# Kernel tuning notes

Measured on AMD Instinct MI355X. Metric: run time of the kernel, lower is better.

## Reference

```python
import jax, jax.numpy as jnp
import numpy as np
import math

B, H, S, D = 2, 16, 2048, 128
COEFF = 2.0  # layer_number


def setup_inputs() -> dict:
    key = jax.random.key(0)
    kq, kk, kv = jax.random.split(key, 3)
    return {
        "query_layer": jax.random.normal(kq, (B, H, S, D), dtype=jnp.float32),
        "key_layer": jax.random.normal(kk, (B, H, S, D), dtype=jnp.float32),
        "value_layer": jax.random.normal(kv, (B, H, S, D), dtype=jnp.float32),
    }


def reference(query_layer, key_layer, value_layer):
    b, h, sq, d = query_layer.shape
    sk = key_layer.shape[2]
    norm_factor = math.sqrt(d) * COEFF
    # raw scores [b,h,sq,sk]; divide by sqrt(d)*coeff, cast fp32, multiply by coeff
    scores = jnp.einsum("bhqd,bhkd->bhqk", query_layer, key_layer) / norm_factor
    scores = scores.astype(jnp.float32) * COEFF
    # causal mask (sq == sk path with attention_mask=None)
    causal = jnp.tril(jnp.ones((sq, sk), dtype=bool))
    scores = jnp.where(causal, scores, jnp.float32(-jnp.inf))
    probs = jax.nn.softmax(scores, axis=-1).astype(value_layer.dtype)
    # dropout p=0.0 -> identity
    ctx = jnp.einsum("bhqk,bhkd->bhqd", probs, value_layer)
    # [b,h,sq,d] -> [b,sq,h*d]
    return ctx.transpose(0, 2, 1, 3).reshape(b, sq, h * d)
```

## Files before the change

kernel.cpp:

```cpp
#include <hip/hip_runtime.h>
#include <hip/hip_bf16.h>
#include <math.h>

#define NB 2
#define NH 16
#define NS 2048
#define ND 128

typedef __bf16 bf16x8 __attribute__((ext_vector_type(8)));
typedef float f32x16 __attribute__((ext_vector_type(16)));

__global__ __launch_bounds__(256)
void prep(const float* __restrict__ K, const float* __restrict__ V,
          char* __restrict__ Kb, char* __restrict__ Vb)
{
    if (blockIdx.x < 4096) {
        int g = blockIdx.x * 256 + threadIdx.x;
        const int c8 = g & 15;
        const int row = g >> 4;
        const int s = row & 2047, bh = row >> 11;
        const int jt = s >> 6, r = s & 63;
        const float* src = K + ((size_t)row << 7) + (c8 << 3);
        float4 a = *(const float4*)src;
        float4 c = *(const float4*)(src + 4);
        bf16x8 o;
        o[0]=(__bf16)a.x; o[1]=(__bf16)a.y; o[2]=(__bf16)a.z; o[3]=(__bf16)a.w;
        o[4]=(__bf16)c.x; o[5]=(__bf16)c.y; o[6]=(__bf16)c.z; o[7]=(__bf16)c.w;
        *(bf16x8*)(Kb + (((size_t)(bh*32 + jt)) << 14) + r*256 + ((c8 ^ (r & 15)) << 4)) = o;
    } else {
        const int T    = blockIdx.x - 4096;
        const int w2   = threadIdx.x >> 6;
        const int lane = threadIdx.x & 63;
        const float2* vbase = (const float2*)V + ((size_t)T << 12);
        char* ob = Vb + ((size_t)T << 14);
        #pragma unroll
        for (int p = 0; p < 2; ++p) {
            const int kv8 = w2*2 + p;
            bf16x8 o0, o1;
            #pragma unroll
            for (int j = 0; j < 8; ++j) {
                float2 x = vbase[(size_t)(kv8*8 + j)*64 + lane];
                o0[j] = (__bf16)x.x;
                o1[j] = (__bf16)x.y;
            }
            *(bf16x8*)(ob + lane*256 + ((kv8 ^ (lane & 15)) << 4))       = o0;
            *(bf16x8*)(ob + lane*256 + (((8 | kv8) ^ (lane & 15)) << 4)) = o1;
        }
    }
}

__device__ __forceinline__ void gld16(void* lds, const void* gsrc)
{
    __builtin_amdgcn_global_load_lds(
        (const __attribute__((address_space(1))) void*)gsrc,
        (__attribute__((address_space(3))) void*)lds, 16, 0, 0);
}

__global__ __launch_bounds__(256, 2)
void fa_fwd(const float* __restrict__ Qg_, const char* __restrict__ Kb,
            const char* __restrict__ Vb, float* __restrict__ Out)
{
    __shared__ char lds_[65536];

    const int tid  = threadIdx.x;
    const int w    = tid >> 6;
    const int lane = tid & 63;
    const int l31  = lane & 31;
    const int h    = lane >> 5;

    const int c  = blockIdx.x;
    const int bh = c & 31;
    const int qt = (c < 256) ? (c >> 5) : (23 - (c >> 5));
    const int b  = bh >> 4, head = bh & 15;
    const int nt = 2 * (qt + 1);
    const int qb = qt * 128;
    const int qw = qb + 32 * w;

    const float* Qg = Qg_ + (size_t)bh * NS * ND;
    const char*  Kt = Kb + ((size_t)bh << 19);
    const char*  Vt = Vb + ((size_t)bh << 19);

    int kaddr[8], vaddr[4];
    #pragma unroll
    for (int ks = 0; ks < 8; ++ks)
        kaddr[ks] = l31*256 + (((2*ks + h) ^ (lane & 15)) << 4);
    #pragma unroll
    for (int ks = 0; ks < 4; ++ks)
        vaddr[ks] = (l31 >> 1)*256 + (((((lane & 1) << 3) | (2*ks + h)) ^ (l31 >> 1)) << 4);

    auto stage = [&](int t, int buf) {
        const char* kg = Kt + (((size_t)t) << 14) + tid*16;
        const char* vg = Vt + (((size_t)t) << 14) + tid*16;
        char* kl = lds_ + buf*16384 + w*1024;
        char* vl = lds_ + 32768 + buf*16384 + w*1024;
        #pragma unroll
        for (int i = 0; i < 4; ++i) gld16(kl + i*4096, kg + i*4096);
        #pragma unroll
        for (int i = 0; i < 4; ++i) gld16(vl + i*4096, vg + i*4096);
    };

    stage(0, 0);
    stage(1, 1);

    const float CSC = 0.08838834764831845f * 1.4426950408889634f;
    bf16x8 qf[8];
    {
        const float* qrow = Qg + (size_t)(qb + 32*w + l31) * ND + 8*h;
        #pragma unroll
        for (int ks = 0; ks < 8; ++ks) {
            float4 a = *(const float4*)(qrow + 16*ks);
            float4 d = *(const float4*)(qrow + 16*ks + 4);
            bf16x8 f;
            f[0]=(__bf16)(a.x*CSC); f[1]=(__bf16)(a.y*CSC); f[2]=(__bf16)(a.z*CSC); f[3]=(__bf16)(a.w*CSC);
            f[4]=(__bf16)(d.x*CSC); f[5]=(__bf16)(d.y*CSC); f[6]=(__bf16)(d.z*CSC); f[7]=(__bf16)(d.w*CSC);
            qf[ks] = f;
        }
    }

    f32x16 O_[4];
    #pragma unroll
    for (int db = 0; db < 4; ++db)
        #pragma unroll
        for (int r = 0; r < 16; ++r) O_[db][r] = 0.0f;
    float rs = 0.0f;

    auto compute = [&](int t, int KIMM, int VIMM) {
        f32x16 S0, S1;
        #pragma unroll
        for (int r = 0; r < 16; ++r) { S0[r] = 0.0f; S1[r] = 0.0f; }
        __builtin_amdgcn_s_setprio(1);
        #pragma unroll
        for (int ks = 0; ks < 8; ++ks) {
            bf16x8 ka = *(const bf16x8*)(lds_ + (kaddr[ks] + KIMM));
            bf16x8 kb = *(const bf16x8*)(lds_ + (kaddr[ks] + KIMM + 8192));
            S0 = __builtin_amdgcn_mfma_f32_32x32x16_bf16(ka, qf[ks], S0, 0, 0, 0);
            S1 = __builtin_amdgcn_mfma_f32_32x32x16_bf16(kb, qf[ks], S1, 0, 0, 0);
        }
        __builtin_amdgcn_s_setprio(0);

        if (64*t + 63 > qw) {
            const int limh = qw + l31 - 64*t - 4*h;
            #pragma unroll
            for (int r = 0; r < 16; ++r) {
                const int k0 = (r & 3) + 8*(r >> 2);
                if (k0 > limh)      S0[r] = -INFINITY;
                if (k0 + 32 > limh) S1[r] = -INFINITY;
            }
        }
        #pragma unroll
        for (int r = 0; r < 16; ++r) {
            float e0 = __builtin_amdgcn_exp2f(S0[r]);
            float e1 = __builtin_amdgcn_exp2f(S1[r]);
            rs += e0; rs += e1;
            S0[r] = e0; S1[r] = e1;
        }
        unsigned P0[8], P1[8];
        #pragma unroll
        for (int i = 0; i < 8; ++i) {
            unsigned u0, u1;
            asm("v_cvt_pk_bf16_f32 %0, %1, %2" : "=v"(u0) : "v"(S0[2*i]), "v"(S0[2*i+1]));
            asm("v_cvt_pk_bf16_f32 %0, %1, %2" : "=v"(u1) : "v"(S1[2*i]), "v"(S1[2*i+1]));
            P0[i] = u0; P1[i] = u1;
        }
        bf16x8 pa[4];
        #pragma unroll
        for (int ks = 0; ks < 4; ++ks) {
            const int o = 4*(ks & 1);
            unsigned a0, a1, b0, b1;
            if (ks < 2) { a0 = P0[o]; a1 = P0[o+1]; b0 = P0[o+2]; b1 = P0[o+3]; }
            else        { a0 = P1[o]; a1 = P1[o+1]; b0 = P1[o+2]; b1 = P1[o+3]; }
            asm("v_permlane32_swap_b32 %0, %1" : "+v"(a0), "+v"(b0));
            asm("v_permlane32_swap_b32 %0, %1" : "+v"(a1), "+v"(b1));
            union { unsigned u[4]; bf16x8 v; } cv;
            cv.u[0] = a0; cv.u[1] = a1; cv.u[2] = b0; cv.u[3] = b1;
            pa[ks] = cv.v;
        }
        __builtin_amdgcn_s_setprio(1);
        #pragma unroll
        for (int ks = 0; ks < 4; ++ks)
            #pragma unroll
            for (int db = 0; db < 4; ++db) {
                bf16x8 vf = *(const bf16x8*)(lds_ + (vaddr[ks] + VIMM + db*4096));
                O_[db] = __builtin_amdgcn_mfma_f32_32x32x16_bf16(pa[ks], vf, O_[db], 0, 0, 0);
            }
        __builtin_amdgcn_s_setprio(0);
    };

    for (int t = 0; t < nt; t += 2) {
        asm volatile("s_waitcnt vmcnt(8)" ::: "memory");
        __builtin_amdgcn_s_barrier();
        asm volatile("" ::: "memory");
        if (64*t <= qw + 31) compute(t, 0, 32768);
        asm volatile("" ::: "memory");
        __builtin_amdgcn_s_barrier();
        asm volatile("" ::: "memory");
        if (t + 2 < nt) stage(t + 2, 0);
        if (t + 2 < nt) { asm volatile("s_waitcnt vmcnt(8)" ::: "memory"); }
        else            { asm volatile("s_waitcnt vmcnt(0)" ::: "memory"); }
        __builtin_amdgcn_s_barrier();
        asm volatile("" ::: "memory");
        if (64*(t+1) <= qw + 31) compute(t + 1, 16384, 49152);
        asm volatile("" ::: "memory");
        __builtin_amdgcn_s_barrier();
        asm volatile("" ::: "memory");
        if (t + 3 < nt) stage(t + 3, 1);
    }

    float tot = rs + __shfl_xor(rs, 32, 64);
    float inv = 1.0f / tot;
    float fi[16];
    #pragma unroll
    for (int r = 0; r < 16; ++r)
        fi[r] = __shfl(inv, (r & 3) + 8*(r >> 2) + 4*h, 64);
    float* op = Out + ((size_t)(b*NS + qb + 32*w)) * (NH*ND) + head*ND + l31;
    #pragma unroll
    for (int db = 0; db < 4; ++db)
        #pragma unroll
        for (int r = 0; r < 16; ++r) {
            const int qloc = (r & 3) + 8*(r >> 2) + 4*h;
            op[(size_t)qloc * (NH*ND) + db*32] = O_[db][r] * fi[r];
        }
}

extern "C" void kernel_launch(void* const* d_in, const int* in_sizes, int n_in,
                              void* d_out, int out_size, void* d_ws, size_t ws_size,
                              hipStream_t stream) {
    const float* Q = (const float*)d_in[0];
    const float* K = (const float*)d_in[1];
    const float* V = (const float*)d_in[2];
    float* Out = (float*)d_out;
    char* Kb = (char*)d_ws;
    char* Vb = (char*)d_ws + ((size_t)32 << 19);
    prep<<<dim3(5120), dim3(256), 0, stream>>>(K, V, Kb, Vb);
    fa_fwd<<<dim3(512), dim3(256), 0, stream>>>(Q, Kb, Vb, Out);
}
```

Baseline: 183.3 us.

## Split KV range across two blocks per query tile with flag-synchronized merge

Each query tile's causal KV range is split into two halves processed by separate workgroups (1024 blocks instead of 512). The first half writes unnormalized partial outputs and row sums to workspace and raises a flag; the second half spins on that flag, then merges and normalizes. KV tiles shrink to 32 rows, LDS halves to 32KB and launch bounds allow 4 blocks per CU to raise occupancy. This adds workspace traffic and a spin-wait dependency that could deadlock or stall if the producer block is not resident.

```diff
diff --git a/kernel.cpp b/kernel.cpp
--- a/kernel.cpp
+++ b/kernel.cpp
@@ -10,41 +10,48 @@
 typedef __bf16 bf16x8 __attribute__((ext_vector_type(8)));
 typedef float f32x16 __attribute__((ext_vector_type(16)));
 
+#define PART_STRIDE 66560
+
 __global__ __launch_bounds__(256)
 void prep(const float* __restrict__ K, const float* __restrict__ V,
-          char* __restrict__ Kb, char* __restrict__ Vb)
+          char* __restrict__ Kb, char* __restrict__ Vb, int* __restrict__ F)
 {
     if (blockIdx.x < 4096) {
+        if (blockIdx.x == 0) { F[threadIdx.x] = 0; F[256 + threadIdx.x] = 0; }
         int g = blockIdx.x * 256 + threadIdx.x;
         const int c8 = g & 15;
         const int row = g >> 4;
         const int s = row & 2047, bh = row >> 11;
-        const int jt = s >> 6, r = s & 63;
+        const int jt = s >> 5, r = s & 31;
         const float* src = K + ((size_t)row << 7) + (c8 << 3);
         float4 a = *(const float4*)src;
         float4 c = *(const float4*)(src + 4);
         bf16x8 o;
         o[0]=(__bf16)a.x; o[1]=(__bf16)a.y; o[2]=(__bf16)a.z; o[3]=(__bf16)a.w;
         o[4]=(__bf16)c.x; o[5]=(__bf16)c.y; o[6]=(__bf16)c.z; o[7]=(__bf16)c.w;
-        *(bf16x8*)(Kb + (((size_t)(bh*32 + jt)) << 14) + r*256 + ((c8 ^ (r & 15)) << 4)) = o;
+        *(bf16x8*)(Kb + (((size_t)(bh*64 + jt)) << 13) + r*256 + ((c8 ^ (r & 15)) << 4)) = o;
     } else {
-        const int T    = blockIdx.x - 4096;
-        const int w2   = threadIdx.x >> 6;
-        const int lane = threadIdx.x & 63;
-        const float2* vbase = (const float2*)V + ((size_t)T << 12);
-        char* ob = Vb + ((size_t)T << 14);
-        #pragma unroll
-        for (int p = 0; p < 2; ++p) {
-            const int kv8 = w2*2 + p;
-            bf16x8 o0, o1;
+        const int T  = blockIdx.x - 4096;
+        const int dq = threadIdx.x & 31;
+        const int u  = threadIdx.x >> 5;
+        const int jt_sub = u >> 2, kv8 = u & 3;
+        const float4* vb4 = (const float4*)V + ((size_t)T << 11);
+        char* ob = Vb + ((size_t)T << 14) + jt_sub*8192;
+        float4 xx[8];
+        #pragma unroll
+        for (int j = 0; j < 8; ++j) xx[j] = vb4[(size_t)(u*8 + j)*32 + dq];
+        #pragma unroll
+        for (int dd = 0; dd < 4; ++dd) {
+            bf16x8 o;
             #pragma unroll
             for (int j = 0; j < 8; ++j) {
-                float2 x = vbase[(size_t)(kv8*8 + j)*64 + lane];
-                o0[j] = (__bf16)x.x;
-                o1[j] = (__bf16)x.y;
-            }
-            *(bf16x8*)(ob + lane*256 + ((kv8 ^ (lane & 15)) << 4))       = o0;
-            *(bf16x8*)(ob + lane*256 + (((8 | kv8) ^ (lane & 15)) << 4)) = o1;
+                float v = (dd == 0) ? xx[j].x : (dd == 1) ? xx[j].y
+                        : (dd == 2) ? xx[j].z : xx[j].w;
+                o[j] = (__bf16)v;
+            }
+            const int rp = 2*dq + (dd >> 1);
+            const int slot = (((dd & 1) << 2) | kv8) ^ (rp & 7);
+            *(bf16x8*)(ob + rp*128 + (slot << 4)) = o;
         }
     }
 }
@@ -56,11 +63,12 @@
         (__attribute__((address_space(3))) void*)lds, 16, 0, 0);
 }
 
-__global__ __launch_bounds__(256, 2)
+__global__ __launch_bounds__(256, 4)
 void fa_fwd(const float* __restrict__ Qg_, const char* __restrict__ Kb,
-            const char* __restrict__ Vb, float* __restrict__ Out)
+            const char* __restrict__ Vb, float* __restrict__ Part,
+            int* __restrict__ F, float* __restrict__ Out)
 {
-    __shared__ char lds_[65536];
+    __shared__ char lds_[32768];
 
     const int tid  = threadIdx.x;
     const int w    = tid >> 6;
@@ -70,37 +78,41 @@
 
     const int c  = blockIdx.x;
     const int bh = c & 31;
-    const int qt = (c < 256) ? (c >> 5) : (23 - (c >> 5));
+    const int a  = (c >> 5) & 3;
+    const int hf = (c >> 7) & 1;
+    const int c8 = c >> 8;
+    const int qt = (c8 == 0) ? 15 - 2*a : (c8 == 1) ? 2*a
+                 : (c8 == 2) ? 14 - 2*a : 2*a + 1;
     const int b  = bh >> 4, head = bh & 15;
-    const int nt = 2 * (qt + 1);
-    const int qb = qt * 128;
-    const int qw = qb + 32 * w;
+    const int nt  = 2 * (qt + 1);
+    const int jt0 = hf * nt;
+    const int qb  = qt * 128;
+    const int qw  = qb + 32 * w;
+    const int pair = bh * 16 + qt;
 
     const float* Qg = Qg_ + (size_t)bh * NS * ND;
     const char*  Kt = Kb + ((size_t)bh << 19);
     const char*  Vt = Vb + ((size_t)bh << 19);
 
-    int kaddr[8], vaddr[4];
+    int kaddr[8], vaddr[2];
     #pragma unroll
     for (int ks = 0; ks < 8; ++ks)
-        kaddr[ks] = l31*256 + (((2*ks + h) ^ (lane & 15)) << 4);
-    #pragma unroll
-    for (int ks = 0; ks < 4; ++ks)
-        vaddr[ks] = (l31 >> 1)*256 + (((((lane & 1) << 3) | (2*ks + h)) ^ (l31 >> 1)) << 4);
-
-    auto stage = [&](int t, int buf) {
-        const char* kg = Kt + (((size_t)t) << 14) + tid*16;
-        const char* vg = Vt + (((size_t)t) << 14) + tid*16;
-        char* kl = lds_ + buf*16384 + w*1024;
-        char* vl = lds_ + 32768 + buf*16384 + w*1024;
-        #pragma unroll
-        for (int i = 0; i < 4; ++i) gld16(kl + i*4096, kg + i*4096);
-        #pragma unroll
-        for (int i = 0; i < 4; ++i) gld16(vl + i*4096, vg + i*4096);
+        kaddr[ks] = l31*256 + (((2*ks + h) ^ (l31 & 15)) << 4);
+    #pragma unroll
+    for (int ks = 0; ks < 2; ++ks)
+        vaddr[ks] = (l31 >> 1)*128 + (((((lane & 1) << 2) | (2*ks + h)) ^ ((l31 >> 1) & 7)) << 4);
+
+    auto stage = [&](int jt, int buf) {
+        const char* kg = Kt + (((size_t)jt) << 13) + w*2048 + lane*16;
+        const char* vg = Vt + (((size_t)jt) << 13) + w*2048 + lane*16;
+        char* kl = lds_ + buf*8192 + w*2048;
+        char* vl = lds_ + 16384 + buf*8192 + w*2048;
+        gld16(kl, kg); gld16(kl + 1024, kg + 1024);
+        gld16(vl, vg); gld16(vl + 1024, vg + 1024);
     };
 
-    stage(0, 0);
-    stage(1, 1);
+    stage(jt0, 0);
+    stage(jt0 + 1, 1);
 
     const float CSC = 0.08838834764831845f * 1.4426950408889634f;
     bf16x8 qf[8];
@@ -108,10 +120,10 @@
         const float* qrow = Qg + (size_t)(qb + 32*w + l31) * ND + 8*h;
         #pragma unroll
         for (int ks = 0; ks < 8; ++ks) {
-            float4 a = *(const float4*)(qrow + 16*ks);
+            float4 x = *(const float4*)(qrow + 16*ks);
             float4 d = *(const float4*)(qrow + 16*ks + 4);
             bf16x8 f;
-            f[0]=(__bf16)(a.x*CSC); f[1]=(__bf16)(a.y*CSC); f[2]=(__bf16)(a.z*CSC); f[3]=(__bf16)(a.w*CSC);
+            f[0]=(__bf16)(x.x*CSC); f[1]=(__bf16)(x.y*CSC); f[2]=(__bf16)(x.z*CSC); f[3]=(__bf16)(x.w*CSC);
             f[4]=(__bf16)(d.x*CSC); f[5]=(__bf16)(d.y*CSC); f[6]=(__bf16)(d.z*CSC); f[7]=(__bf16)(d.w*CSC);
             qf[ks] = f;
         }
@@ -124,51 +136,45 @@
         for (int r = 0; r < 16; ++r) O_[db][r] = 0.0f;
     float rs = 0.0f;
 
-    auto compute = [&](int t, int KIMM, int VIMM) {
-        f32x16 S0, S1;
-        #pragma unroll
-        for (int r = 0; r < 16; ++r) { S0[r] = 0.0f; S1[r] = 0.0f; }
+    auto compute = [&](int jt, int KIMM, int VIMM) {
+        bf16x8 kf[8];
+        #pragma unroll
+        for (int ks = 0; ks < 8; ++ks)
+            kf[ks] = *(const bf16x8*)(lds_ + (kaddr[ks] + KIMM));
+        f32x16 S;
+        #pragma unroll
+        for (int r = 0; r < 16; ++r) S[r] = 0.0f;
         __builtin_amdgcn_s_setprio(1);
         #pragma unroll
-        for (int ks = 0; ks < 8; ++ks) {
-            bf16x8 ka = *(const bf16x8*)(lds_ + (kaddr[ks] + KIMM));
-            bf16x8 kb = *(const bf16x8*)(lds_ + (kaddr[ks] + KIMM + 8192));
-            S0 = __builtin_amdgcn_mfma_f32_32x32x16_bf16(ka, qf[ks], S0, 0, 0, 0);
-            S1 = __builtin_amdgcn_mfma_f32_32x32x16_bf16(kb, qf[ks], S1, 0, 0, 0);
-        }
+        for (int ks = 0; ks < 8; ++ks)
+            S = __builtin_amdgcn_mfma_f32_32x32x16_bf16(kf[ks], qf[ks], S, 0, 0, 0);
         __builtin_amdgcn_s_setprio(0);
 
-        if (64*t + 63 > qw) {
-            const int limh = qw + l31 - 64*t - 4*h;
+        if (32*jt + 31 > qw) {
+            const int limh = qw + l31 - 32*jt - 4*h;
             #pragma unroll
             for (int r = 0; r < 16; ++r) {
                 const int k0 = (r & 3) + 8*(r >> 2);
-                if (k0 > limh)      S0[r] = -INFINITY;
-                if (k0 + 32 > limh) S1[r] = -INFINITY;
+                if (k0 > limh) S[r] = -INFINITY;
             }
         }
         #pragma unroll
         for (int r = 0; r < 16; ++r) {
-            float e0 = __builtin_amdgcn_exp2f(S0[r]);
-            float e1 = __builtin_amdgcn_exp2f(S1[r]);
-            rs += e0; rs += e1;
-            S0[r] = e0; S1[r] = e1;
-        }
-        unsigned P0[8], P1[8];
+            float e = __builtin_amdgcn_exp2f(S[r]);
+            rs += e;
+            S[r] = e;
+        }
+        unsigned P0[8];
         #pragma unroll
         for (int i = 0; i < 8; ++i) {
-            unsigned u0, u1;
-            asm("v_cvt_pk_bf16_f32 %0, %1, %2" : "=v"(u0) : "v"(S0[2*i]), "v"(S0[2*i+1]));
-            asm("v_cvt_pk_bf16_f32 %0, %1, %2" : "=v"(u1) : "v"(S1[2*i]), "v"(S1[2*i+1]));
-            P0[i] = u0; P1[i] = u1;
-        }
-        bf16x8 pa[4];
-        #pragma unroll
-        for (int ks = 0; ks < 4; ++ks) {
-            const int o = 4*(ks & 1);
-            unsigned a0, a1, b0, b1;
-            if (ks < 2) { a0 = P0[o]; a1 = P0[o+1]; b0 = P0[o+2]; b1 = P0[o+3]; }
-            else        { a0 = P1[o]; a1 = P1[o+1]; b0 = P1[o+2]; b1 = P1[o+3]; }
+            unsigned u0;
+            asm("v_cvt_pk_bf16_f32 %0, %1, %2" : "=v"(u0) : "v"(S[2*i]), "v"(S[2*i+1]));
+            P0[i] = u0;
+        }
+        bf16x8 pa[2];
+        #pragma unroll
+        for (int ks = 0; ks < 2; ++ks) {
+            unsigned a0 = P0[4*ks], a1 = P0[4*ks+1], b0 = P0[4*ks+2], b1 = P0[4*ks+3];
             asm("v_permlane32_swap_b32 %0, %1" : "+v"(a0), "+v"(b0));
             asm("v_permlane32_swap_b32 %0, %1" : "+v"(a1), "+v"(b1));
             union { unsigned u[4]; bf16x8 v; } cv;
@@ -177,37 +183,64 @@
         }
         __builtin_amdgcn_s_setprio(1);
         #pragma unroll
-        for (int ks = 0; ks < 4; ++ks)
+        for (int ks = 0; ks < 2; ++ks)
             #pragma unroll
             for (int db = 0; db < 4; ++db) {
-                bf16x8 vf = *(const bf16x8*)(lds_ + (vaddr[ks] + VIMM + db*4096));
+                bf16x8 vf = *(const bf16x8*)(lds_ + (vaddr[ks] + VIMM + db*2048));
                 O_[db] = __builtin_amdgcn_mfma_f32_32x32x16_bf16(pa[ks], vf, O_[db], 0, 0, 0);
             }
         __builtin_amdgcn_s_setprio(0);
     };
 
     for (int t = 0; t < nt; t += 2) {
-        asm volatile("s_waitcnt vmcnt(8)" ::: "memory");
-        __builtin_amdgcn_s_barrier();
-        asm volatile("" ::: "memory");
-        if (64*t <= qw + 31) compute(t, 0, 32768);
-        asm volatile("" ::: "memory");
-        __builtin_amdgcn_s_barrier();
-        asm volatile("" ::: "memory");
-        if (t + 2 < nt) stage(t + 2, 0);
-        if (t + 2 < nt) { asm volatile("s_waitcnt vmcnt(8)" ::: "memory"); }
+        asm volatile("s_waitcnt vmcnt(4)" ::: "memory");
+        __builtin_amdgcn_s_barrier();
+        asm volatile("" ::: "memory");
+        if (32*(jt0 + t) <= qw + 31) compute(jt0 + t, 0, 16384);
+        asm volatile("" ::: "memory");
+        __builtin_amdgcn_s_barrier();
+        asm volatile("" ::: "memory");
+        if (t + 2 < nt) stage(jt0 + t + 2, 0);
+        if (t + 2 < nt) { asm volatile("s_waitcnt vmcnt(4)" ::: "memory"); }
         else            { asm volatile("s_waitcnt vmcnt(0)" ::: "memory"); }
         __builtin_amdgcn_s_barrier();
         asm volatile("" ::: "memory");
-        if (64*(t+1) <= qw + 31) compute(t + 1, 16384, 49152);
-        asm volatile("" ::: "memory");
-        __builtin_amdgcn_s_barrier();
-        asm volatile("" ::: "memory");
-        if (t + 3 < nt) stage(t + 3, 1);
+        if (32*(jt0 + t + 1) <= qw + 31) compute(jt0 + t + 1, 8192, 24576);
+        asm volatile("" ::: "memory");
+        __builtin_amdgcn_s_barrier();
+        asm volatile("" ::: "memory");
+        if (t + 2 < nt) stage(jt0 + t + 3, 1);
     }
 
     float tot = rs + __shfl_xor(rs, 32, 64);
-    float inv = 1.0f / tot;
+    float* PO = (float*)((char*)Part + (size_t)pair * PART_STRIDE);
+    float* PR = PO + 128*128;
+
+    if (hf == 0) {
+        #pragma unroll
+        for (int db = 0; db < 4; ++db)
+            #pragma unroll
+            for (int r = 0; r < 16; ++r) {
+                const int qloc = (r & 3) + 8*(r >> 2) + 4*h;
+                PO[(size_t)(32*w + qloc)*128 + db*32 + l31] = O_[db][r];
+            }
+        if (h == 0) PR[32*w + l31] = tot;
+        __threadfence();
+        __syncthreads();
+        if (tid == 0)
+            __hip_atomic_store(F + pair, 1, __ATOMIC_RELEASE, __HIP_MEMORY_SCOPE_AGENT);
+        return;
+    }
+
+    if (tid == 0) {
+        while (__hip_atomic_load(F + pair, __ATOMIC_ACQUIRE, __HIP_MEMORY_SCOPE_AGENT) == 0)
+            __builtin_amdgcn_s_sleep(2);
+    }
+    __syncthreads();
+    __threadfence();
+
+    float rsp = PR[32*w + l31];
+    float inv = 1.0f / (tot + rsp);
     float fi[16];
     #pragma unroll
     for (int r = 0; r < 16; ++r)
@@ -218,7 +251,8 @@
         #pragma unroll
         for (int r = 0; r < 16; ++r) {
             const int qloc = (r & 3) + 8*(r >> 2) + 4*h;
-            op[(size_t)qloc * (NH*ND) + db*32] = O_[db][r] * fi[r];
+            float part = PO[(size_t)(32*w + qloc)*128 + db*32 + l31];
+            op[(size_t)qloc * (NH*ND) + db*32] = (O_[db][r] + part) * fi[r];
         }
 }
 
@@ -230,7 +264,9 @@
     const float* V = (const float*)d_in[2];
     float* Out = (float*)d_out;
     char* Kb = (char*)d_ws;
-    char* Vb = (char*)d_ws + ((size_t)32 << 19);
-    prep<<<dim3(5120), dim3(256), 0, stream>>>(K, V, Kb, Vb);
-    fa_fwd<<<dim3(512), dim3(256), 0, stream>>>(Q, Kb, Vb, Out);
-}
+    char* Vb = (char*)d_ws + ((size_t)16 << 20);
+    float* Part = (float*)((char*)d_ws + ((size_t)32 << 20));
+    int* F = (int*)((char*)d_ws + ((size_t)32 << 20) + 512*(size_t)PART_STRIDE);
+    prep<<<dim3(5120), dim3(256), 0, stream>>>(K, V, Kb, Vb, F);
+    fa_fwd<<<dim3(1024), dim3(256), 0, stream>>>(Q, Kb, Vb, Part, F, Out);
+}
```

After: 438.3 us. 2.39x slower.
